# Optimization experiments

Hardware: AMD Instinct MI355X
Metric: run time of the kernel (lower is better)

The kernel has to match this reference:

```python
import jax, jax.numpy as jnp
import numpy as np

N, D, B, C, T, TOD = 8192, 32, 2, 8, 12, 288
PARAM_SCALE = 0.3  # keep relu+softmax logits well-conditioned (original uses plain randn init)


def setup_inputs() -> dict:
    key = jax.random.key(0)
    k0, k1, k2, k3, k4 = jax.random.split(key, 5)
    return {
        "x": jax.random.normal(k0, (B, C, N, T), dtype=jnp.float32),
        "nodevec1": PARAM_SCALE * jax.random.normal(k1, (N, D), dtype=jnp.float32),
        "nodevec2": PARAM_SCALE * jax.random.normal(k2, (N, D), dtype=jnp.float32),
        "timevec": PARAM_SCALE * jax.random.normal(k3, (TOD, D), dtype=jnp.float32),
        "k": PARAM_SCALE * jax.random.normal(k4, (D, D, D), dtype=jnp.float32),
        "time_ind": 100,
    }


def reference(x, nodevec1, nodevec2, timevec, k, time_ind):
    # Dynamic Tucker-decomposition adjacency (SpatialGraphConv.forward, eval mode -> dropout is identity)
    tv = timevec[time_ind]                             # [D]   time_vec
    core = jnp.einsum('d,def->ef', tv, k)              # [D,D] adp1 (squeezed)
    # adp2/adp3 chain: (nodevec1 @ core) @ nodevec2.T  -> [N,N]
    adp = jnp.einsum('ne,ef->nf', nodevec1, core)      # [N,D]
    adp = jnp.einsum('nf,mf->nm', adp, nodevec2)       # [N,N]
    adp = jax.nn.softmax(jax.nn.relu(adp), axis=-1)    # row-softmax over neighbors
    # NConv: neighbor aggregation  'bcnt,nm->bcmt'
    return jnp.einsum('bcnt,nm->bcmt', x, adp)
```

## Files before the change

kernel.cpp:

```cpp
#include <hip/hip_runtime.h>
#include <hip/hip_bf16.h>


#define NN 8192
#define DD 32
#define TT 12
#define NSPLIT 8
#define CHUNK 1024

typedef __attribute__((ext_vector_type(8))) short bf16x8;
typedef __attribute__((ext_vector_type(4))) float f32x4;
typedef __attribute__((ext_vector_type(4))) unsigned int u32x4;

static __device__ __forceinline__ unsigned short f2bf(float f) {
  unsigned int u = __float_as_uint(f);
  u = (u + 0x7FFFu + ((u >> 16) & 1u)) >> 16;
  return (unsigned short)u;
}

static __device__ __forceinline__ float fexp2(float x) {
#if __has_builtin(__builtin_amdgcn_exp2f)
  return __builtin_amdgcn_exp2f(x);
#else
  return __builtin_exp2f(x);
#endif
}

#define MFMA32(A, B, C) __builtin_amdgcn_mfma_f32_16x16x32_bf16((A), (B), (C), 0, 0, 0)

static __device__ __forceinline__ unsigned int pk_rne(float a, float b) {
  unsigned int ua = __float_as_uint(a);
  unsigned int ub = __float_as_uint(b);
  ua = ua + 0x7FFFu + ((ua >> 16) & 1u);
  ub = ub + 0x7FFFu + ((ub >> 16) & 1u);
  return (ua >> 16) | (ub & 0xFFFF0000u);
}

static __device__ __forceinline__ bf16x8 relu_exp2_pack(f32x4 lo, f32x4 hi) {
  u32x4 t;
  t[0] = pk_rne(fexp2(fmaxf(lo[0], 0.f)), fexp2(fmaxf(lo[1], 0.f)));
  t[1] = pk_rne(fexp2(fmaxf(lo[2], 0.f)), fexp2(fmaxf(lo[3], 0.f)));
  t[2] = pk_rne(fexp2(fmaxf(hi[0], 0.f)), fexp2(fmaxf(hi[1], 0.f)));
  t[3] = pk_rne(fexp2(fmaxf(hi[2], 0.f)), fexp2(fmaxf(hi[3], 0.f)));
  return __builtin_bit_cast(bf16x8, t);
}

__global__ __launch_bounds__(256) void k_prep(const float* __restrict__ nv1,
                                              const float* __restrict__ nv2,
                                              const float* __restrict__ timevec,
                                              const float* __restrict__ kk,
                                              const int* __restrict__ tind,
                                              unsigned short* __restrict__ t1b,
                                              unsigned short* __restrict__ nv2b,
                                              float* __restrict__ sums) {
  __shared__ float cs[1024];
  const int tid = threadIdx.x;
  if (tid < 128) sums[blockIdx.x * 128 + tid] = 0.f;
  const float* tv = timevec + (size_t)tind[0] * DD;
  for (int idx = tid; idx < 1024; idx += 256) {
    float acc = 0.f;
#pragma unroll
    for (int d = 0; d < DD; ++d) acc += tv[d] * kk[d * 1024 + idx];
    cs[idx] = acc;
  }
  __syncthreads();
  const int nbase = blockIdx.x * 128;
  const int f = tid & 31, sub = tid >> 5;
#pragma unroll 4
  for (int it = 0; it < 16; ++it) {
    const int n = nbase + it * 8 + sub;
    const float* nr = nv1 + (size_t)n * DD;
    float acc = 0.f;
#pragma unroll
    for (int e = 0; e < DD; ++e) acc += nr[e] * cs[e * DD + f];
    t1b[(size_t)n * DD + f] = f2bf(acc * 1.4426950408889634f);
  }
#pragma unroll 4
  for (int it = 0; it < 16; ++it) {
    const int idx = nbase * DD + it * 256 + tid;
    nv2b[idx] = f2bf(nv2[idx]);
  }
}

__global__ __launch_bounds__(256) void k_stats(const unsigned short* __restrict__ t1b,
                                               const unsigned short* __restrict__ nv2b,
                                               float* __restrict__ sums) {
  const int tid = threadIdx.x;
  const int w = tid >> 6, lane = tid & 63, q = lane >> 4, i16 = lane & 15;
  const int nbase = blockIdx.x * 64 + w * 16;
  bf16x8 a = *(const bf16x8*)(t1b + (size_t)(nbase + i16) * DD + q * 8);
  const f32x4 z4 = {0.f, 0.f, 0.f, 0.f};
  float s[4] = {0.f, 0.f, 0.f, 0.f};
  const int m0 = blockIdx.y * 1024;
  for (int mt = m0; mt < m0 + 1024; mt += 64) {
#pragma unroll
    for (int u = 0; u < 4; ++u) {
      bf16x8 b = *(const bf16x8*)(nv2b + (size_t)(mt + u * 16 + i16) * DD + q * 8);
      f32x4 d = __builtin_amdgcn_mfma_f32_16x16x32_bf16(a, b, z4, 0, 0, 0);
#pragma unroll
      for (int r = 0; r < 4; ++r) s[r] += fexp2(fmaxf(d[r], 0.f));
    }
  }
#pragma unroll
  for (int r = 0; r < 4; ++r)
    for (int off = 1; off < 16; off <<= 1) s[r] += __shfl_xor(s[r], off, 64);
  if (i16 == 0) {
#pragma unroll
    for (int r = 0; r < 4; ++r) atomicAdd(&sums[nbase + q * 4 + r], s[r]);
  }
}

__global__ __launch_bounds__(256) void k_y(const float* __restrict__ x,
                                           const float* __restrict__ sums,
                                           unsigned short* __restrict__ yT) {
  __shared__ float xs[3328];
  const int tid = threadIdx.x;
  const int n0 = blockIdx.x * 256;
  const int bc = blockIdx.y;
  const float* xp = x + (size_t)bc * NN * TT + (size_t)n0 * TT;
#pragma unroll
  for (int j = 0; j < 12; ++j) {
    const int idx = j * 256 + tid;
    xs[(idx / 12) * 13 + idx % 12] = xp[idx];
  }
  __syncthreads();
  const float rinv = 1.0f / sums[n0 + tid];
#pragma unroll
  for (int t = 0; t < 12; ++t)
    yT[(size_t)(bc * TT + t) * NN + n0 + tid] = f2bf(xs[tid * 13 + t] * rinv);
}

__global__ __launch_bounds__(256, 3) void k_mega(const unsigned short* __restrict__ t1b,
                                                 const unsigned short* __restrict__ nv2b,
                                                 const unsigned short* __restrict__ yT,
                                                 float* __restrict__ part) {
  const int tid = threadIdx.x;
  const int w = tid >> 6, lane = tid & 63, q = lane >> 4, i16 = lane & 15;
  const int mb = blockIdx.x * 64;
  const int nt0 = blockIdx.y * CHUNK;

  bf16x8 bg[4];
#pragma unroll
  for (int ms = 0; ms < 4; ++ms)
    bg[ms] = *(const bf16x8*)(nv2b + (size_t)(mb + ms * 16 + i16) * DD + q * 8);

  f32x4 acc[3][4];
#pragma unroll
  for (int c = 0; c < 3; ++c)
#pragma unroll
    for (int ms = 0; ms < 4; ++ms) acc[c][ms] = (f32x4){0.f, 0.f, 0.f, 0.f};

  const int perm = ((i16 >> 2) << 3) | (i16 & 3);
  const unsigned short* tp = t1b + (size_t)(nt0 + perm) * DD + q * 8;
  const unsigned short* yp0 = yT + (size_t)((w * 3 + 0) * 16 + i16) * NN + nt0 + q * 8;
  const unsigned short* yp1 = yp0 + (size_t)16 * NN;
  const unsigned short* yp2 = yp1 + (size_t)16 * NN;

  const f32x4 z4 = {0.f, 0.f, 0.f, 0.f};

  bf16x8 alo = *(const bf16x8*)tp;
  bf16x8 ahi = *(const bf16x8*)(tp + 4 * DD);
  bf16x8 e[4];
#pragma unroll
  for (int ms = 0; ms < 4; ++ms) {
    f32x4 dlo = MFMA32(alo, bg[ms], z4);
    f32x4 dhi = MFMA32(ahi, bg[ms], z4);
    e[ms] = relu_exp2_pack(dlo, dhi);
  }
  bf16x8 y0 = *(const bf16x8*)yp0;
  bf16x8 y1 = *(const bf16x8*)yp1;
  bf16x8 y2 = *(const bf16x8*)yp2;
  alo = *(const bf16x8*)(tp + 32 * DD);
  ahi = *(const bf16x8*)(tp + 36 * DD);

  for (int sl = 1; sl < 32; ++sl) {
    const int o = sl * 32;
    bf16x8 y0n = *(const bf16x8*)(yp0 + o);
    bf16x8 y1n = *(const bf16x8*)(yp1 + o);
    bf16x8 y2n = *(const bf16x8*)(yp2 + o);
    bf16x8 alo_n = *(const bf16x8*)(tp + (size_t)(o + 32) * DD);
    bf16x8 ahi_n = *(const bf16x8*)(tp + (size_t)(o + 36) * DD);

    f32x4 d00 = MFMA32(alo, bg[0], z4);
    f32x4 d01 = MFMA32(ahi, bg[0], z4);
    f32x4 d10 = MFMA32(alo, bg[1], z4);
    f32x4 d11 = MFMA32(ahi, bg[1], z4);
    acc[0][0] = MFMA32(y0, e[0], acc[0][0]);
    acc[1][0] = MFMA32(y1, e[0], acc[1][0]);
    acc[2][0] = MFMA32(y2, e[0], acc[2][0]);
    acc[0][1] = MFMA32(y0, e[1], acc[0][1]);
    acc[1][1] = MFMA32(y1, e[1], acc[1][1]);
    acc[2][1] = MFMA32(y2, e[1], acc[2][1]);
    e[0] = relu_exp2_pack(d00, d01);
    e[1] = relu_exp2_pack(d10, d11);

    f32x4 d20 = MFMA32(alo, bg[2], z4);
    f32x4 d21 = MFMA32(ahi, bg[2], z4);
    f32x4 d30 = MFMA32(alo, bg[3], z4);
    f32x4 d31 = MFMA32(ahi, bg[3], z4);
    acc[0][2] = MFMA32(y0, e[2], acc[0][2]);
    acc[1][2] = MFMA32(y1, e[2], acc[1][2]);
    acc[2][2] = MFMA32(y2, e[2], acc[2][2]);
    acc[0][3] = MFMA32(y0, e[3], acc[0][3]);
    acc[1][3] = MFMA32(y1, e[3], acc[1][3]);
    acc[2][3] = MFMA32(y2, e[3], acc[2][3]);
    e[2] = relu_exp2_pack(d20, d21);
    e[3] = relu_exp2_pack(d30, d31);

    y0 = y0n; y1 = y1n; y2 = y2n;
    alo = alo_n; ahi = ahi_n;
  }

#pragma unroll
  for (int ms = 0; ms < 4; ++ms) {
    acc[0][ms] = MFMA32(y0, e[ms], acc[0][ms]);
    acc[1][ms] = MFMA32(y1, e[ms], acc[1][ms]);
    acc[2][ms] = MFMA32(y2, e[ms], acc[2][ms]);
  }

  float* pp = part + (size_t)blockIdx.y * 192 * NN;
#pragma unroll
  for (int c = 0; c < 3; ++c)
#pragma unroll
    for (int ms = 0; ms < 4; ++ms) {
      const int colbase = (w * 3 + c) * 16 + q * 4;
      const int m = mb + ms * 16 + i16;
#pragma unroll
      for (int r = 0; r < 4; ++r)
        pp[(size_t)(colbase + r) * NN + m] = acc[c][ms][r];
    }
}

__global__ __launch_bounds__(256) void k_reduce(const float* __restrict__ part,
                                                float* __restrict__ out) {
  __shared__ float os[3328];
  const int tid = threadIdx.x;
  const int m0 = blockIdx.x * 256;
  const int bc = blockIdx.y;
#pragma unroll
  for (int t = 0; t < 12; ++t) {
    const int col = bc * TT + t;
    float s = 0.f;
#pragma unroll
    for (int nc = 0; nc < NSPLIT; ++nc)
      s += part[((size_t)nc * 192 + col) * NN + m0 + tid];
    os[tid * 13 + t] = s;
  }
  __syncthreads();
  float* op = out + (size_t)bc * NN * TT + (size_t)m0 * TT;
#pragma unroll
  for (int j = 0; j < 12; ++j) {
    const int idx = j * 256 + tid;
    op[idx] = os[(idx / 12) * 13 + idx % 12];
  }
}

extern "C" void kernel_launch(void* const* d_in, const int* in_sizes, int n_in,
                              void* d_out, int out_size, void* d_ws, size_t ws_size,
                              hipStream_t stream) {
  const float* x = (const float*)d_in[0];
  const float* nv1 = (const float*)d_in[1];
  const float* nv2 = (const float*)d_in[2];
  const float* tv = (const float*)d_in[3];
  const float* kk = (const float*)d_in[4];
  const int* tind = (const int*)d_in[5];
  float* out = (float*)d_out;

  char* ws = (char*)d_ws;
  unsigned short* t1b  = (unsigned short*)(ws);
  unsigned short* nv2b = (unsigned short*)(ws + 524288);
  float* sums          = (float*)(ws + 1048576);
  unsigned short* yT   = (unsigned short*)(ws + 1081344);
  float* part          = (float*)(ws + 4227072);

  k_prep<<<64, 256, 0, stream>>>(nv1, nv2, tv, kk, tind, t1b, nv2b, sums);
  k_stats<<<dim3(128, 8), 256, 0, stream>>>(t1b, nv2b, sums);
  k_y<<<dim3(32, 16), 256, 0, stream>>>(x, sums, yT);
  k_mega<<<dim3(128, NSPLIT), 256, 0, stream>>>(t1b, nv2b, yT, part);
  k_reduce<<<dim3(32, 16), 256, 0, stream>>>(part, out);
}
```

Measured before the change: 184.3 us.

## Give each wave all 192 output columns over 32 rows to cut exp recomputation

```diff
diff --git a/kernel.cpp b/kernel.cpp
--- a/kernel.cpp
+++ b/kernel.cpp
@@ -130,101 +130,69 @@
     yT[(size_t)(bc * TT + t) * NN + n0 + tid] = f2bf(xs[tid * 13 + t] * rinv);
 }
 
-__global__ __launch_bounds__(256, 3) void k_mega(const unsigned short* __restrict__ t1b,
+__global__ __launch_bounds__(256, 2) void k_mega(const unsigned short* __restrict__ t1b,
                                                  const unsigned short* __restrict__ nv2b,
                                                  const unsigned short* __restrict__ yT,
                                                  float* __restrict__ part) {
   const int tid = threadIdx.x;
   const int w = tid >> 6, lane = tid & 63, q = lane >> 4, i16 = lane & 15;
-  const int mb = blockIdx.x * 64;
+  const int mw = blockIdx.x * 128 + w * 32;
   const int nt0 = blockIdx.y * CHUNK;
 
-  bf16x8 bg[4];
-#pragma unroll
-  for (int ms = 0; ms < 4; ++ms)
-    bg[ms] = *(const bf16x8*)(nv2b + (size_t)(mb + ms * 16 + i16) * DD + q * 8);
-
-  f32x4 acc[3][4];
-#pragma unroll
-  for (int c = 0; c < 3; ++c)
-#pragma unroll
-    for (int ms = 0; ms < 4; ++ms) acc[c][ms] = (f32x4){0.f, 0.f, 0.f, 0.f};
+  bf16x8 bg[2];
+#pragma unroll
+  for (int ms = 0; ms < 2; ++ms)
+    bg[ms] = *(const bf16x8*)(nv2b + (size_t)(mw + ms * 16 + i16) * DD + q * 8);
+
+  f32x4 acc[12][2];
+#pragma unroll
+  for (int c = 0; c < 12; ++c)
+#pragma unroll
+    for (int ms = 0; ms < 2; ++ms) acc[c][ms] = (f32x4){0.f, 0.f, 0.f, 0.f};
 
   const int perm = ((i16 >> 2) << 3) | (i16 & 3);
-  const unsigned short* tp = t1b + (size_t)(nt0 + perm) * DD + q * 8;
-  const unsigned short* yp0 = yT + (size_t)((w * 3 + 0) * 16 + i16) * NN + nt0 + q * 8;
-  const unsigned short* yp1 = yp0 + (size_t)16 * NN;
-  const unsigned short* yp2 = yp1 + (size_t)16 * NN;
+  const unsigned short* tcur = t1b + (size_t)(nt0 + perm) * DD + q * 8;
+  int yoff = i16 * NN + nt0 + q * 8;
 
   const f32x4 z4 = {0.f, 0.f, 0.f, 0.f};
 
-  bf16x8 alo = *(const bf16x8*)tp;
-  bf16x8 ahi = *(const bf16x8*)(tp + 4 * DD);
-  bf16x8 e[4];
-#pragma unroll
-  for (int ms = 0; ms < 4; ++ms) {
-    f32x4 dlo = MFMA32(alo, bg[ms], z4);
-    f32x4 dhi = MFMA32(ahi, bg[ms], z4);
-    e[ms] = relu_exp2_pack(dlo, dhi);
-  }
-  bf16x8 y0 = *(const bf16x8*)yp0;
-  bf16x8 y1 = *(const bf16x8*)yp1;
-  bf16x8 y2 = *(const bf16x8*)yp2;
-  alo = *(const bf16x8*)(tp + 32 * DD);
-  ahi = *(const bf16x8*)(tp + 36 * DD);
-
-  for (int sl = 1; sl < 32; ++sl) {
-    const int o = sl * 32;
-    bf16x8 y0n = *(const bf16x8*)(yp0 + o);
-    bf16x8 y1n = *(const bf16x8*)(yp1 + o);
-    bf16x8 y2n = *(const bf16x8*)(yp2 + o);
-    bf16x8 alo_n = *(const bf16x8*)(tp + (size_t)(o + 32) * DD);
-    bf16x8 ahi_n = *(const bf16x8*)(tp + (size_t)(o + 36) * DD);
+  bf16x8 alo = *(const bf16x8*)tcur;
+  bf16x8 ahi = *(const bf16x8*)(tcur + 4 * DD);
+
+  for (int it = 0; it < 32; ++it) {
+    bf16x8 y[12];
+#pragma unroll
+    for (int c = 0; c < 12; ++c)
+      y[c] = *(const bf16x8*)(yT + (size_t)(c * 16) * NN + yoff);
+
+    const unsigned short* tnext = tcur + 32 * DD;
+    bf16x8 alo_n = *(const bf16x8*)tnext;
+    bf16x8 ahi_n = *(const bf16x8*)(tnext + 4 * DD);
 
     f32x4 d00 = MFMA32(alo, bg[0], z4);
     f32x4 d01 = MFMA32(ahi, bg[0], z4);
     f32x4 d10 = MFMA32(alo, bg[1], z4);
     f32x4 d11 = MFMA32(ahi, bg[1], z4);
-    acc[0][0] = MFMA32(y0, e[0], acc[0][0]);
-    acc[1][0] = MFMA32(y1, e[0], acc[1][0]);
-    acc[2][0] = MFMA32(y2, e[0], acc[2][0]);
-    acc[0][1] = MFMA32(y0, e[1], acc[0][1]);
-    acc[1][1] = MFMA32(y1, e[1], acc[1][1]);
-    acc[2][1] = MFMA32(y2, e[1], acc[2][1]);
-    e[0] = relu_exp2_pack(d00, d01);
-    e[1] = relu_exp2_pack(d10, d11);
-
-    f32x4 d20 = MFMA32(alo, bg[2], z4);
-    f32x4 d21 = MFMA32(ahi, bg[2], z4);
-    f32x4 d30 = MFMA32(alo, bg[3], z4);
-    f32x4 d31 = MFMA32(ahi, bg[3], z4);
-    acc[0][2] = MFMA32(y0, e[2], acc[0][2]);
-    acc[1][2] = MFMA32(y1, e[2], acc[1][2]);
-    acc[2][2] = MFMA32(y2, e[2], acc[2][2]);
-    acc[0][3] = MFMA32(y0, e[3], acc[0][3]);
-    acc[1][3] = MFMA32(y1, e[3], acc[1][3]);
-    acc[2][3] = MFMA32(y2, e[3], acc[2][3]);
-    e[2] = relu_exp2_pack(d20, d21);
-    e[3] = relu_exp2_pack(d30, d31);
-
-    y0 = y0n; y1 = y1n; y2 = y2n;
+
+    bf16x8 e0 = relu_exp2_pack(d00, d01);
+#pragma unroll
+    for (int c = 0; c < 12; ++c) acc[c][0] = MFMA32(y[c], e0, acc[c][0]);
+    bf16x8 e1 = relu_exp2_pack(d10, d11);
+#pragma unroll
+    for (int c = 0; c < 12; ++c) acc[c][1] = MFMA32(y[c], e1, acc[c][1]);
+
     alo = alo_n; ahi = ahi_n;
-  }
-
-#pragma unroll
-  for (int ms = 0; ms < 4; ++ms) {
-    acc[0][ms] = MFMA32(y0, e[ms], acc[0][ms]);
-    acc[1][ms] = MFMA32(y1, e[ms], acc[1][ms]);
-    acc[2][ms] = MFMA32(y2, e[ms], acc[2][ms]);
+    tcur = tnext;
+    yoff += 32;
   }
 
   float* pp = part + (size_t)blockIdx.y * 192 * NN;
 #pragma unroll
-  for (int c = 0; c < 3; ++c)
-#pragma unroll
-    for (int ms = 0; ms < 4; ++ms) {
-      const int colbase = (w * 3 + c) * 16 + q * 4;
-      const int m = mb + ms * 16 + i16;
+  for (int c = 0; c < 12; ++c)
+#pragma unroll
+    for (int ms = 0; ms < 2; ++ms) {
+      const int colbase = c * 16 + q * 4;
+      const int m = mw + ms * 16 + i16;
 #pragma unroll
       for (int r = 0; r < 4; ++r)
         pp[(size_t)(colbase + r) * NN + m] = acc[c][ms][r];
@@ -276,6 +244,6 @@
   k_prep<<<64, 256, 0, stream>>>(nv1, nv2, tv, kk, tind, t1b, nv2b, sums);
   k_stats<<<dim3(128, 8), 256, 0, stream>>>(t1b, nv2b, sums);
   k_y<<<dim3(32, 16), 256, 0, stream>>>(x, sums, yT);
-  k_mega<<<dim3(128, NSPLIT), 256, 0, stream>>>(t1b, nv2b, yT, part);
+  k_mega<<<dim3(64, NSPLIT), 256, 0, stream>>>(t1b, nv2b, yT, part);
   k_reduce<<<dim3(32, 16), 256, 0, stream>>>(part, out);
 }
```

New measurement: 210.5 us. 14.2% more time.
